# Optimization experiments

Hardware: AMD Instinct MI355X
Metric: run time of the kernel (lower is better)

## Reference

```python
import jax, jax.numpy as jnp
import numpy as np

QMIN, QMAX = -128.0, 127.0  # 8-bit signed activation range


def fq_act(x, s):
    """Fake-quantize activations: clip(round(x/s))*s with straight-through estimator."""
    y = jnp.clip(jnp.round(x / s), QMIN, QMAX) * s
    return x + jax.lax.stop_gradient(y - x)


def fq_weight(w):
    """Per-tensor max-abs symmetric (narrow-range) 8-bit weight fake-quant with STE."""
    s = jnp.max(jnp.abs(w)) / 127.0
    y = jnp.clip(jnp.round(w / s), -127.0, 127.0) * s
    return w + jax.lax.stop_gradient(y - w)


def conv1x1(x, w, b):
    # x: [b,c,h,w], w: [o,c] -> [b,o,h,w]
    return jnp.einsum('bchw,oc->bohw', x, w) + b[None, :, None, None]


def setup_inputs() -> dict:
    key = jax.random.key(0)
    ks = jax.random.split(key, 6)
    B, C, HC, H, W = 8, 64, 32, 64, 64
    x = jax.random.normal(ks[0], (B, C, H, W), dtype=jnp.float32)
    wq = jax.random.normal(ks[1], (HC, C), dtype=jnp.float32) * 0.05
    wk = jax.random.normal(ks[2], (HC, C), dtype=jnp.float32) * 0.05
    wv = jax.random.normal(ks[3], (HC, C), dtype=jnp.float32) * 0.05
    wp = jax.random.normal(ks[4], (C, HC), dtype=jnp.float32) * 0.05
    return {
        'x': x,
        'wq': wq, 'bq': jnp.zeros((HC,), jnp.float32),
        'wk': wk, 'bk': jnp.zeros((HC,), jnp.float32),
        'wv': wv, 'bv': jnp.zeros((HC,), jnp.float32),
        'wp': wp, 'bp': jnp.zeros((C,), jnp.float32),
        's_in': jnp.ones((1,), jnp.float32) * 0.0625,
        's_out': jnp.ones((1,), jnp.float32) * 0.0625,
    }


def reference(x, wq, bq, wk, bk, wv, bv, wp, bp, s_in, s_out):
    b, c, h, w = x.shape
    hc = wq.shape[0]
    n = h * w
    xq = fq_act(x, s_in)                              # quant_inp(x)
    q = conv1x1(xq, fq_weight(wq), bq).reshape(b, hc, n).transpose(0, 2, 1)  # [b,n,hc]
    k = conv1x1(xq, fq_weight(wk), bk).reshape(b, hc, n)                     # [b,hc,n]
    v = conv1x1(xq, fq_weight(wv), bv).reshape(b, hc, n).transpose(0, 2, 1)  # [b,n,hc]
    z = jax.nn.softmax(jnp.einsum('bqc,bck->bqk', q, k), axis=-1)            # [b,n,n]
    z = jnp.einsum('bqk,bkc->bqc', z, v).transpose(0, 2, 1).reshape(b, hc, h, w)
    z = fq_act(z, s_in)                               # quant_inp(z) (shared module/scale)
    out = xq + conv1x1(z, fq_weight(wp), bp)
    return fq_act(out, s_out)                         # self.act QuantIdentity
```

## Files before the change

### kernel.cpp

```cpp
#include <hip/hip_runtime.h>
#include <hip/hip_bf16.h>
#include <cstdint>
#include <cstddef>

#define NB 8
#define NC 64
#define NHC 32
#define NN 4096
#define LOG2E 1.44269504088896340736f

typedef short v8s __attribute__((ext_vector_type(8)));
typedef float v4f __attribute__((ext_vector_type(4)));

__device__ __forceinline__ unsigned short f2b(float f) {
    unsigned int u = __builtin_bit_cast(unsigned int, f);
    u += 0x7fffu + ((u >> 16) & 1u);
    return (unsigned short)(u >> 16);
}
__device__ __forceinline__ float b2f(unsigned short s) {
    unsigned int u = ((unsigned int)s) << 16;
    return __builtin_bit_cast(float, u);
}
__device__ __forceinline__ unsigned int pack2_bf16(float a, float b) {
    unsigned int ua = __builtin_bit_cast(unsigned int, a);
    ua += 0x7fffu + ((ua >> 16) & 1u);
    unsigned int ub = __builtin_bit_cast(unsigned int, b);
    ub += 0x7fffu + ((ub >> 16) & 1u);
    return (ua >> 16) | (ub & 0xffff0000u);
}
__device__ __forceinline__ unsigned int trunc2_bf16(float a, float b) {
    return __builtin_amdgcn_perm(__builtin_bit_cast(unsigned int, b),
                                 __builtin_bit_cast(unsigned int, a), 0x07060302u);
}

__global__ __launch_bounds__(256) void k_qkv(
    const float* __restrict__ x,
    const float* __restrict__ wq, const float* __restrict__ wk, const float* __restrict__ wv,
    const float* __restrict__ bq, const float* __restrict__ bk, const float* __restrict__ bv,
    const float* __restrict__ s_in,
    unsigned short* __restrict__ xqb, unsigned short* __restrict__ qb,
    unsigned short* __restrict__ kb, unsigned short* __restrict__ vb)
{
    int blk = blockIdx.x;
    int b   = blk >> 6;
    int p0  = (blk & 63) * 64;
    int tid = threadIdx.x;

    __shared__ __align__(16) unsigned short xt[64][72];
    __shared__ __align__(16) unsigned short wlds[6144];
    __shared__ float red[3][256];

    float4 q0 = *(const float4*)(wq + tid * 8), q1 = *(const float4*)(wq + tid * 8 + 4);
    float4 k0 = *(const float4*)(wk + tid * 8), k1 = *(const float4*)(wk + tid * 8 + 4);
    float4 v0 = *(const float4*)(wv + tid * 8), v1 = *(const float4*)(wv + tid * 8 + 4);
    float mq = fmaxf(fmaxf(fmaxf(fabsf(q0.x), fabsf(q0.y)), fmaxf(fabsf(q0.z), fabsf(q0.w))),
                     fmaxf(fmaxf(fabsf(q1.x), fabsf(q1.y)), fmaxf(fabsf(q1.z), fabsf(q1.w))));
    float mk = fmaxf(fmaxf(fmaxf(fabsf(k0.x), fabsf(k0.y)), fmaxf(fabsf(k0.z), fabsf(k0.w))),
                     fmaxf(fmaxf(fabsf(k1.x), fabsf(k1.y)), fmaxf(fabsf(k1.z), fabsf(k1.w))));
    float mv = fmaxf(fmaxf(fmaxf(fabsf(v0.x), fabsf(v0.y)), fmaxf(fabsf(v0.z), fabsf(v0.w))),
                     fmaxf(fmaxf(fabsf(v1.x), fabsf(v1.y)), fmaxf(fabsf(v1.z), fabsf(v1.w))));
    red[0][tid] = mq; red[1][tid] = mk; red[2][tid] = mv;
    __syncthreads();
    for (int s = 128; s > 0; s >>= 1) {
        if (tid < s) {
            red[0][tid] = fmaxf(red[0][tid], red[0][tid + s]);
            red[1][tid] = fmaxf(red[1][tid], red[1][tid + s]);
            red[2][tid] = fmaxf(red[2][tid], red[2][tid + s]);
        }
        __syncthreads();
    }
    float sq = red[0][0] / 127.0f, sk = red[1][0] / 127.0f, sw = red[2][0] / 127.0f;
    {
        const float* srcs[3] = {wq, wk, wv};
        float scl[3] = {sq, sk, sw};
        #pragma unroll
        for (int t = 0; t < 3; ++t) {
            #pragma unroll
            for (int j = 0; j < 8; ++j) {
                float val = srcs[t][tid * 8 + j];
                float r = fminf(fmaxf(rintf(val / scl[t]), -127.f), 127.f);
                wlds[t * 2048 + tid * 8 + j] = f2b(r * scl[t]);
            }
        }
    }

    float sv = s_in[0];
    float sinv = 1.0f / sv;
    int jj = tid & 15;
    int c0 = tid >> 4;
    #pragma unroll
    for (int it = 0; it < 4; ++it) {
        int c = c0 + it * 16;
        size_t gi = ((size_t)(b * NC + c) << 12) + p0 + jj * 4;
        float4 xv = *(const float4*)(x + gi);
        float r0 = fminf(fmaxf(rintf(xv.x * sinv), -128.f), 127.f) * sv;
        float r1 = fminf(fmaxf(rintf(xv.y * sinv), -128.f), 127.f) * sv;
        float r2 = fminf(fmaxf(rintf(xv.z * sinv), -128.f), 127.f) * sv;
        float r3 = fminf(fmaxf(rintf(xv.w * sinv), -128.f), 127.f) * sv;
        *(uint2*)(xqb + gi) = make_uint2(pack2_bf16(r0, r1), pack2_bf16(r2, r3));
        xt[jj * 4 + 0][c] = f2b(r0);
        xt[jj * 4 + 1][c] = f2b(r1);
        xt[jj * 4 + 2][c] = f2b(r2);
        xt[jj * 4 + 3][c] = f2b(r3);
    }
    __syncthreads();

    int wave = tid >> 6;
    int lane = tid & 63;
    int quad = lane >> 4;
    int l15  = lane & 15;

    v8s bf0 = *(const v8s*)(&xt[wave * 16 + l15][0  + quad * 8]);
    v8s bf1 = *(const v8s*)(&xt[wave * 16 + l15][32 + quad * 8]);

    int pos = p0 + wave * 16 + l15;
    size_t posg = (size_t)b * NN + pos;
    const v4f zc = {0.f, 0.f, 0.f, 0.f};

    #pragma unroll
    for (int rb = 0; rb < 6; ++rb) {
        v8s a0 = *(const v8s*)(wlds + (rb * 16 + l15) * 64 + 0  + quad * 8);
        v8s a1 = *(const v8s*)(wlds + (rb * 16 + l15) * 64 + 32 + quad * 8);
        v4f t   = __builtin_amdgcn_mfma_f32_16x16x32_bf16(a0, bf0, zc, 0, 0, 0);
        v4f acc = __builtin_amdgcn_mfma_f32_16x16x32_bf16(a1, bf1, t, 0, 0, 0);

        int R0 = rb * 16 + quad * 4;
        float vals[4];
        #pragma unroll
        for (int r = 0; r < 4; ++r) {
            int R = R0 + r;
            float bias = (R < 32) ? bq[R] : (R < 64) ? bk[R - 32] : bv[R - 64];
            float vv = acc[r] + bias;
            if (R < 32) vv *= LOG2E;
            vals[r] = vv;
        }
        if (R0 < 32) {
            *(unsigned int*)(qb + posg * NHC + R0)     = pack2_bf16(vals[0], vals[1]);
            *(unsigned int*)(qb + posg * NHC + R0 + 2) = pack2_bf16(vals[2], vals[3]);
        } else if (R0 < 64) {
            *(unsigned int*)(kb + posg * NHC + R0 - 32)     = pack2_bf16(vals[0], vals[1]);
            *(unsigned int*)(kb + posg * NHC + R0 - 32 + 2) = pack2_bf16(vals[2], vals[3]);
        } else {
            #pragma unroll
            for (int r = 0; r < 4; ++r)
                vb[(size_t)(b * NHC + R0 - 64 + r) * NN + pos] = f2b(vals[r]);
        }
    }
}

__global__ __launch_bounds__(256, 2) void k_attn(
    const unsigned short* __restrict__ qb, const unsigned short* __restrict__ kb,
    const unsigned short* __restrict__ vb, const unsigned short* __restrict__ xqb,
    const float* __restrict__ wp, const float* __restrict__ bp,
    const float* __restrict__ s_in, const float* __restrict__ s_out,
    float* __restrict__ out)
{
    int blk  = blockIdx.x;
    int b    = blk >> 6;
    int qt   = blk & 63;
    int qbase = qt * 64;
    int tid  = threadIdx.x;
    int wave = tid >> 6;
    int lane = tid & 63;
    int quad = lane >> 4;
    int l15  = lane & 15;

    __shared__ __align__(16) unsigned short pbuf[4][16 * 72];
    __shared__ __align__(16) float zbuf[4][64][36];
    __shared__ float lbuf[4][64];
    __shared__ __align__(16) unsigned short wpq[2048];
    __shared__ float red[256];

    {
        float4 a0 = *(const float4*)(wp + tid * 8), a1 = *(const float4*)(wp + tid * 8 + 4);
        float mx = fmaxf(fmaxf(fmaxf(fabsf(a0.x), fabsf(a0.y)), fmaxf(fabsf(a0.z), fabsf(a0.w))),
                         fmaxf(fmaxf(fabsf(a1.x), fabsf(a1.y)), fmaxf(fabsf(a1.z), fabsf(a1.w))));
        red[tid] = mx;
        __syncthreads();
        for (int s = 128; s > 0; s >>= 1) {
            if (tid < s) red[tid] = fmaxf(red[tid], red[tid + s]);
            __syncthreads();
        }
        float scale = red[0] / 127.0f;
        float e[8] = {a0.x, a0.y, a0.z, a0.w, a1.x, a1.y, a1.z, a1.w};
        #pragma unroll
        for (int j = 0; j < 8; ++j) {
            float r = fminf(fmaxf(rintf(e[j] / scale), -127.f), 127.f);
            wpq[tid * 8 + j] = f2b(r * scale);
        }
    }

    unsigned short* pb = pbuf[wave];
    const unsigned short* qbat = qb + (size_t)b * NN * NHC;
    const unsigned short* kbat = kb + (size_t)b * NN * NHC;
    const unsigned short* vbat = vb + (size_t)b * NHC * NN;

    v8s qf[4];
    #pragma unroll
    for (int s = 0; s < 4; ++s)
        qf[s] = *(const v8s*)(qbat + (qbase + s * 16 + l15) * NHC + quad * 8);

    const short one_bf16 = (short)0x3F80;
    const v8s ones = {one_bf16, one_bf16, one_bf16, one_bf16,
                      one_bf16, one_bf16, one_bf16, one_bf16};
    const v4f zc = {0.f, 0.f, 0.f, 0.f};
    v4f zt[4][2] = {{zc, zc}, {zc, zc}, {zc, zc}, {zc, zc}};
    v4f lacc[4] = {zc, zc, zc, zc};

    int k0 = wave * 1024;
    const unsigned short* vrow0 = vbat + (size_t)( 0 + l15) * NN;
    const unsigned short* vrow1 = vbat + (size_t)(16 + l15) * NN;

    v8s ck0 = *(const v8s*)(kbat + (k0 +  0 + l15) * NHC + quad * 8);
    v8s ck1 = *(const v8s*)(kbat + (k0 + 16 + l15) * NHC + quad * 8);
    v8s ck2 = *(const v8s*)(kbat + (k0 + 32 + l15) * NHC + quad * 8);
    v8s ck3 = *(const v8s*)(kbat + (k0 + 48 + l15) * NHC + quad * 8);

    for (int i = 0; i < 16; ++i) {
        int cki = k0 + (i << 6);
        int nki = k0 + (((i + 1) & 15) << 6);
        v8s nk0 = *(const v8s*)(kbat + (nki +  0 + l15) * NHC + quad * 8);
        v8s nk1 = *(const v8s*)(kbat + (nki + 16 + l15) * NHC + quad * 8);
        v8s nk2 = *(const v8s*)(kbat + (nki + 32 + l15) * NHC + quad * 8);
        v8s nk3 = *(const v8s*)(kbat + (nki + 48 + l15) * NHC + quad * 8);
        v8s cv0 = *(const v8s*)(vrow0 + cki +  0 + quad * 8);
        v8s cv1 = *(const v8s*)(vrow0 + cki + 32 + quad * 8);
        v8s cv2 = *(const v8s*)(vrow1 + cki +  0 + quad * 8);
        v8s cv3 = *(const v8s*)(vrow1 + cki + 32 + quad * 8);

        #pragma unroll
        for (int s = 0; s < 4; ++s) {
            v4f sa[4];
            sa[0] = __builtin_amdgcn_mfma_f32_16x16x32_bf16(ck0, qf[s], zc, 0, 0, 0);
            sa[1] = __builtin_amdgcn_mfma_f32_16x16x32_bf16(ck1, qf[s], zc, 0, 0, 0);
            sa[2] = __builtin_amdgcn_mfma_f32_16x16x32_bf16(ck2, qf[s], zc, 0, 0, 0);
            sa[3] = __builtin_amdgcn_mfma_f32_16x16x32_bf16(ck3, qf[s], zc, 0, 0, 0);

            #pragma unroll
            for (int t = 0; t < 4; ++t) {
                float p0 = __builtin_amdgcn_exp2f(sa[t][0]);
                float p1 = __builtin_amdgcn_exp2f(sa[t][1]);
                float p2 = __builtin_amdgcn_exp2f(sa[t][2]);
                float p3 = __builtin_amdgcn_exp2f(sa[t][3]);
                *(uint2*)(pb + l15 * 72 + 16 * t + quad * 4) =
                    make_uint2(trunc2_bf16(p0, p1), trunc2_bf16(p2, p3));
            }
            v8s pf0 = *(const v8s*)(pb + l15 * 72 +  0 + quad * 8);
            v8s pf1 = *(const v8s*)(pb + l15 * 72 + 32 + quad * 8);

            zt[s][0] = __builtin_amdgcn_mfma_f32_16x16x32_bf16(cv0, pf0, zt[s][0], 0, 0, 0);
            zt[s][0] = __builtin_amdgcn_mfma_f32_16x16x32_bf16(cv1, pf1, zt[s][0], 0, 0, 0);
            zt[s][1] = __builtin_amdgcn_mfma_f32_16x16x32_bf16(cv2, pf0, zt[s][1], 0, 0, 0);
            zt[s][1] = __builtin_amdgcn_mfma_f32_16x16x32_bf16(cv3, pf1, zt[s][1], 0, 0, 0);
            lacc[s]  = __builtin_amdgcn_mfma_f32_16x16x32_bf16(ones, pf0, lacc[s], 0, 0, 0);
            lacc[s]  = __builtin_amdgcn_mfma_f32_16x16x32_bf16(ones, pf1, lacc[s], 0, 0, 0);
        }
        ck0 = nk0; ck1 = nk1; ck2 = nk2; ck3 = nk3;
    }

    #pragma unroll
    for (int s = 0; s < 4; ++s) {
        *(v4f*)(&zbuf[wave][s * 16 + l15][     quad * 4]) = zt[s][0];
        *(v4f*)(&zbuf[wave][s * 16 + l15][16 + quad * 4]) = zt[s][1];
        if (quad == 0) lbuf[wave][s * 16 + l15] = lacc[s][0];
    }
    __syncthreads();

    int myq = wave * 16 + l15;
    float L = lbuf[0][myq] + lbuf[1][myq] + lbuf[2][myq] + lbuf[3][myq];

    float z[8] = {0.f};
    #pragma unroll
    for (int w = 0; w < 4; ++w) {
        v4f za  = *(const v4f*)(&zbuf[w][myq][quad * 8]);
        v4f zb2 = *(const v4f*)(&zbuf[w][myq][quad * 8 + 4]);
        #pragma unroll
        for (int j = 0; j < 4; ++j) { z[j] += za[j]; z[4 + j] += zb2[j]; }
    }
    float sv = s_in[0], sinv = 1.0f / sv;
    float so = s_out[0], soinv = 1.0f / so;
    float Linv = 1.0f / L;
    unsigned int zp[4];
    #pragma unroll
    for (int jp = 0; jp < 4; ++jp) {
        float a = z[2 * jp]     * Linv;
        float c = z[2 * jp + 1] * Linv;
        a = fminf(fmaxf(rintf(a * sinv), -128.f), 127.f) * sv;
        c = fminf(fmaxf(rintf(c * sinv), -128.f), 127.f) * sv;
        zp[jp] = pack2_bf16(a, c);
    }
    v8s zf = __builtin_bit_cast(v8s, *(uint4*)zp);

    v8s w0f = *(const v8s*)(wpq + ( 0 + l15) * NHC + quad * 8);
    v8s w1f = *(const v8s*)(wpq + (16 + l15) * NHC + quad * 8);
    v8s w2f = *(const v8s*)(wpq + (32 + l15) * NHC + quad * 8);
    v8s w3f = *(const v8s*)(wpq + (48 + l15) * NHC + quad * 8);
    v4f o0 = __builtin_amdgcn_mfma_f32_16x16x32_bf16(w0f, zf, zc, 0, 0, 0);
    v4f o1 = __builtin_amdgcn_mfma_f32_16x16x32_bf16(w1f, zf, zc, 0, 0, 0);
    v4f o2 = __builtin_amdgcn_mfma_f32_16x16x32_bf16(w2f, zf, zc, 0, 0, 0);
    v4f o3 = __builtin_amdgcn_mfma_f32_16x16x32_bf16(w3f, zf, zc, 0, 0, 0);

    int pos = qbase + wave * 16 + l15;
    #pragma unroll
    for (int ot = 0; ot < 4; ++ot) {
        v4f ov = (ot == 0) ? o0 : (ot == 1) ? o1 : (ot == 2) ? o2 : o3;
        #pragma unroll
        for (int r = 0; r < 4; ++r) {
            int oc = ot * 16 + quad * 4 + r;
            size_t idx = (size_t)(b * NC + oc) * NN + pos;
            float val = ov[r] + bp[oc] + b2f(xqb[idx]);
            float f = fminf(fmaxf(rintf(val * soinv), -128.f), 127.f);
            out[idx] = f * so;
        }
    }
}

extern "C" void kernel_launch(void* const* d_in, const int* in_sizes, int n_in,
                              void* d_out, int out_size, void* d_ws, size_t ws_size,
                              hipStream_t stream) {
    const float* x     = (const float*)d_in[0];
    const float* wq    = (const float*)d_in[1];
    const float* bq    = (const float*)d_in[2];
    const float* wk    = (const float*)d_in[3];
    const float* bk    = (const float*)d_in[4];
    const float* wv    = (const float*)d_in[5];
    const float* bv    = (const float*)d_in[6];
    const float* wp    = (const float*)d_in[7];
    const float* bp    = (const float*)d_in[8];
    const float* s_in  = (const float*)d_in[9];
    const float* s_out = (const float*)d_in[10];
    float* out = (float*)d_out;

    char* ws = (char*)d_ws;
    size_t off = 0;
    auto carve = [&](size_t bytes) {
        void* p = ws + off;
        off = (off + bytes + 255) & ~(size_t)255;
        return p;
    };
    unsigned short* xqb = (unsigned short*)carve((size_t)NB * NC * NN * 2);
    unsigned short* qbf = (unsigned short*)carve((size_t)NB * NN * NHC * 2);
    unsigned short* kbf = (unsigned short*)carve((size_t)NB * NN * NHC * 2);
    unsigned short* vbf = (unsigned short*)carve((size_t)NB * NHC * NN * 2);

    hipLaunchKernelGGL(k_qkv, dim3(512), dim3(256), 0, stream,
                       x, wq, wk, wv, bq, bk, bv, s_in, xqb, qbf, kbf, vbf);
    hipLaunchKernelGGL(k_attn, dim3(512), dim3(256), 0, stream,
                       qbf, kbf, vbf, xqb, wp, bp, s_in, s_out, out);
}
```

Baseline: 118.4 us.

## Feed softmax probabilities to PV MFMA from registers via permuted V layout

The attention kernel no longer stages the exponentiated scores through shared memory. It feeds each 16x16 score fragment directly as the B operand of 16x16x16 bf16 MFMAs, and the QKV kernel writes V with a permuted position order so the register layout matches. Block-wide max reductions for the weight scales now use wave shuffles instead of a shared-memory tree with many barriers. The explicit K prefetch double-buffering is removed, and the PV and row-sum work now runs as twice as many smaller MFMAs, which may expose more load latency.

```diff
diff --git a/kernel.cpp b/kernel.cpp
--- a/kernel.cpp
+++ b/kernel.cpp
@@ -10,7 +10,9 @@
 #define LOG2E 1.44269504088896340736f
 
 typedef short v8s __attribute__((ext_vector_type(8)));
+typedef short v4s __attribute__((ext_vector_type(4)));
 typedef float v4f __attribute__((ext_vector_type(4)));
+typedef unsigned int v2u __attribute__((ext_vector_type(2)));
 
 __device__ __forceinline__ unsigned short f2b(float f) {
     unsigned int u = __builtin_bit_cast(unsigned int, f);
@@ -31,6 +33,20 @@
 __device__ __forceinline__ unsigned int trunc2_bf16(float a, float b) {
     return __builtin_amdgcn_perm(__builtin_bit_cast(unsigned int, b),
                                  __builtin_bit_cast(unsigned int, a), 0x07060302u);
+}
+__device__ __forceinline__ float wave_max(float v) {
+    #pragma unroll
+    for (int off = 1; off < 64; off <<= 1) v = fmaxf(v, __shfl_xor(v, off));
+    return v;
+}
+__device__ __forceinline__ v4f mfma16bf16(v4s a, v4s b, v4f c) {
+#if __has_builtin(__builtin_amdgcn_mfma_f32_16x16x16bf16_1k)
+    return __builtin_amdgcn_mfma_f32_16x16x16bf16_1k(a, b, c, 0, 0, 0);
+#else
+    asm volatile("v_mfma_f32_16x16x16_bf16 %0, %1, %2, %0"
+                 : "+v"(c) : "v"(a), "v"(b));
+    return c;
+#endif
 }
 
 __global__ __launch_bounds__(256) void k_qkv(
@@ -45,10 +61,12 @@
     int b   = blk >> 6;
     int p0  = (blk & 63) * 64;
     int tid = threadIdx.x;
+    int wave = tid >> 6;
+    int lane = tid & 63;
 
     __shared__ __align__(16) unsigned short xt[64][72];
     __shared__ __align__(16) unsigned short wlds[6144];
-    __shared__ float red[3][256];
+    __shared__ float red[3][4];
 
     float4 q0 = *(const float4*)(wq + tid * 8), q1 = *(const float4*)(wq + tid * 8 + 4);
     float4 k0 = *(const float4*)(wk + tid * 8), k1 = *(const float4*)(wk + tid * 8 + 4);
@@ -59,28 +77,21 @@
                      fmaxf(fmaxf(fabsf(k1.x), fabsf(k1.y)), fmaxf(fabsf(k1.z), fabsf(k1.w))));
     float mv = fmaxf(fmaxf(fmaxf(fabsf(v0.x), fabsf(v0.y)), fmaxf(fabsf(v0.z), fabsf(v0.w))),
                      fmaxf(fmaxf(fabsf(v1.x), fabsf(v1.y)), fmaxf(fabsf(v1.z), fabsf(v1.w))));
-    red[0][tid] = mq; red[1][tid] = mk; red[2][tid] = mv;
+    mq = wave_max(mq); mk = wave_max(mk); mv = wave_max(mv);
+    if (lane == 0) { red[0][wave] = mq; red[1][wave] = mk; red[2][wave] = mv; }
     __syncthreads();
-    for (int s = 128; s > 0; s >>= 1) {
-        if (tid < s) {
-            red[0][tid] = fmaxf(red[0][tid], red[0][tid + s]);
-            red[1][tid] = fmaxf(red[1][tid], red[1][tid + s]);
-            red[2][tid] = fmaxf(red[2][tid], red[2][tid + s]);
-        }
-        __syncthreads();
-    }
-    float sq = red[0][0] / 127.0f, sk = red[1][0] / 127.0f, sw = red[2][0] / 127.0f;
+    float sq = fmaxf(fmaxf(red[0][0], red[0][1]), fmaxf(red[0][2], red[0][3])) / 127.0f;
+    float sk = fmaxf(fmaxf(red[1][0], red[1][1]), fmaxf(red[1][2], red[1][3])) / 127.0f;
+    float sw = fmaxf(fmaxf(red[2][0], red[2][1]), fmaxf(red[2][2], red[2][3])) / 127.0f;
     {
-        const float* srcs[3] = {wq, wk, wv};
-        float scl[3] = {sq, sk, sw};
-        #pragma unroll
-        for (int t = 0; t < 3; ++t) {
-            #pragma unroll
-            for (int j = 0; j < 8; ++j) {
-                float val = srcs[t][tid * 8 + j];
-                float r = fminf(fmaxf(rintf(val / scl[t]), -127.f), 127.f);
-                wlds[t * 2048 + tid * 8 + j] = f2b(r * scl[t]);
-            }
+        float eq[8] = {q0.x, q0.y, q0.z, q0.w, q1.x, q1.y, q1.z, q1.w};
+        float ek[8] = {k0.x, k0.y, k0.z, k0.w, k1.x, k1.y, k1.z, k1.w};
+        float ev[8] = {v0.x, v0.y, v0.z, v0.w, v1.x, v1.y, v1.z, v1.w};
+        #pragma unroll
+        for (int j = 0; j < 8; ++j) {
+            wlds[0 * 2048 + tid * 8 + j] = f2b(fminf(fmaxf(rintf(eq[j] / sq), -127.f), 127.f) * sq);
+            wlds[1 * 2048 + tid * 8 + j] = f2b(fminf(fmaxf(rintf(ek[j] / sk), -127.f), 127.f) * sk);
+            wlds[2 * 2048 + tid * 8 + j] = f2b(fminf(fmaxf(rintf(ev[j] / sw), -127.f), 127.f) * sw);
         }
     }
 
@@ -105,8 +116,6 @@
     }
     __syncthreads();
 
-    int wave = tid >> 6;
-    int lane = tid & 63;
     int quad = lane >> 4;
     int l15  = lane & 15;
 
@@ -115,6 +124,7 @@
 
     int pos = p0 + wave * 16 + l15;
     size_t posg = (size_t)b * NN + pos;
+    int posP = p0 + (l15 >> 2) * 16 + wave * 4 + (l15 & 3);
     const v4f zc = {0.f, 0.f, 0.f, 0.f};
 
     #pragma unroll
@@ -143,7 +153,7 @@
         } else {
             #pragma unroll
             for (int r = 0; r < 4; ++r)
-                vb[(size_t)(b * NHC + R0 - 64 + r) * NN + pos] = f2b(vals[r]);
+                vb[(size_t)(b * NHC + R0 - 64 + r) * NN + posP] = f2b(vals[r]);
         }
     }
 }
@@ -165,23 +175,19 @@
     int quad = lane >> 4;
     int l15  = lane & 15;
 
-    __shared__ __align__(16) unsigned short pbuf[4][16 * 72];
     __shared__ __align__(16) float zbuf[4][64][36];
     __shared__ float lbuf[4][64];
     __shared__ __align__(16) unsigned short wpq[2048];
-    __shared__ float red[256];
+    __shared__ float redw[4];
 
     {
         float4 a0 = *(const float4*)(wp + tid * 8), a1 = *(const float4*)(wp + tid * 8 + 4);
         float mx = fmaxf(fmaxf(fmaxf(fabsf(a0.x), fabsf(a0.y)), fmaxf(fabsf(a0.z), fabsf(a0.w))),
                          fmaxf(fmaxf(fabsf(a1.x), fabsf(a1.y)), fmaxf(fabsf(a1.z), fabsf(a1.w))));
-        red[tid] = mx;
+        mx = wave_max(mx);
+        if (lane == 0) redw[wave] = mx;
         __syncthreads();
-        for (int s = 128; s > 0; s >>= 1) {
-            if (tid < s) red[tid] = fmaxf(red[tid], red[tid + s]);
-            __syncthreads();
-        }
-        float scale = red[0] / 127.0f;
+        float scale = fmaxf(fmaxf(redw[0], redw[1]), fmaxf(redw[2], redw[3])) / 127.0f;
         float e[8] = {a0.x, a0.y, a0.z, a0.w, a1.x, a1.y, a1.z, a1.w};
         #pragma unroll
         for (int j = 0; j < 8; ++j) {
@@ -190,7 +196,6 @@
         }
     }
 
-    unsigned short* pb = pbuf[wave];
     const unsigned short* qbat = qb + (size_t)b * NN * NHC;
     const unsigned short* kbat = kb + (size_t)b * NN * NHC;
     const unsigned short* vbat = vb + (size_t)b * NHC * NN;
@@ -200,9 +205,8 @@
     for (int s = 0; s < 4; ++s)
         qf[s] = *(const v8s*)(qbat + (qbase + s * 16 + l15) * NHC + quad * 8);
 
-    const short one_bf16 = (short)0x3F80;
-    const v8s ones = {one_bf16, one_bf16, one_bf16, one_bf16,
-                      one_bf16, one_bf16, one_bf16, one_bf16};
+    const short ob = (short)0x3F80;
+    const v4s ones4 = {ob, ob, ob, ob};
     const v4f zc = {0.f, 0.f, 0.f, 0.f};
     v4f zt[4][2] = {{zc, zc}, {zc, zc}, {zc, zc}, {zc, zc}};
     v4f lacc[4] = {zc, zc, zc, zc};
@@ -211,22 +215,25 @@
     const unsigned short* vrow0 = vbat + (size_t)( 0 + l15) * NN;
     const unsigned short* vrow1 = vbat + (size_t)(16 + l15) * NN;
 
-    v8s ck0 = *(const v8s*)(kbat + (k0 +  0 + l15) * NHC + quad * 8);
-    v8s ck1 = *(const v8s*)(kbat + (k0 + 16 + l15) * NHC + quad * 8);
-    v8s ck2 = *(const v8s*)(kbat + (k0 + 32 + l15) * NHC + quad * 8);
-    v8s ck3 = *(const v8s*)(kbat + (k0 + 48 + l15) * NHC + quad * 8);
-
     for (int i = 0; i < 16; ++i) {
         int cki = k0 + (i << 6);
-        int nki = k0 + (((i + 1) & 15) << 6);
-        v8s nk0 = *(const v8s*)(kbat + (nki +  0 + l15) * NHC + quad * 8);
-        v8s nk1 = *(const v8s*)(kbat + (nki + 16 + l15) * NHC + quad * 8);
-        v8s nk2 = *(const v8s*)(kbat + (nki + 32 + l15) * NHC + quad * 8);
-        v8s nk3 = *(const v8s*)(kbat + (nki + 48 + l15) * NHC + quad * 8);
-        v8s cv0 = *(const v8s*)(vrow0 + cki +  0 + quad * 8);
-        v8s cv1 = *(const v8s*)(vrow0 + cki + 32 + quad * 8);
-        v8s cv2 = *(const v8s*)(vrow1 + cki +  0 + quad * 8);
-        v8s cv3 = *(const v8s*)(vrow1 + cki + 32 + quad * 8);
+        v8s ck0 = *(const v8s*)(kbat + (cki +  0 + l15) * NHC + quad * 8);
+        v8s ck1 = *(const v8s*)(kbat + (cki + 16 + l15) * NHC + quad * 8);
+        v8s ck2 = *(const v8s*)(kbat + (cki + 32 + l15) * NHC + quad * 8);
+        v8s ck3 = *(const v8s*)(kbat + (cki + 48 + l15) * NHC + quad * 8);
+        v8s v00 = *(const v8s*)(vrow0 + cki + quad * 16);
+        v8s v01 = *(const v8s*)(vrow0 + cki + quad * 16 + 8);
+        v8s v10 = *(const v8s*)(vrow1 + cki + quad * 16);
+        v8s v11 = *(const v8s*)(vrow1 + cki + quad * 16 + 8);
+        v4s va[2][4];
+        va[0][0] = __builtin_shufflevector(v00, v00, 0, 1, 2, 3);
+        va[0][1] = __builtin_shufflevector(v00, v00, 4, 5, 6, 7);
+        va[0][2] = __builtin_shufflevector(v01, v01, 0, 1, 2, 3);
+        va[0][3] = __builtin_shufflevector(v01, v01, 4, 5, 6, 7);
+        va[1][0] = __builtin_shufflevector(v10, v10, 0, 1, 2, 3);
+        va[1][1] = __builtin_shufflevector(v10, v10, 4, 5, 6, 7);
+        va[1][2] = __builtin_shufflevector(v11, v11, 0, 1, 2, 3);
+        va[1][3] = __builtin_shufflevector(v11, v11, 4, 5, 6, 7);
 
         #pragma unroll
         for (int s = 0; s < 4; ++s) {
@@ -238,24 +245,17 @@
 
             #pragma unroll
             for (int t = 0; t < 4; ++t) {
-                float p0 = __builtin_amdgcn_exp2f(sa[t][0]);
-                float p1 = __builtin_amdgcn_exp2f(sa[t][1]);
-                float p2 = __builtin_amdgcn_exp2f(sa[t][2]);
-                float p3 = __builtin_amdgcn_exp2f(sa[t][3]);
-                *(uint2*)(pb + l15 * 72 + 16 * t + quad * 4) =
-                    make_uint2(trunc2_bf16(p0, p1), trunc2_bf16(p2, p3));
+                v2u w;
+                w.x = trunc2_bf16(__builtin_amdgcn_exp2f(sa[t][0]),
+                                  __builtin_amdgcn_exp2f(sa[t][1]));
+                w.y = trunc2_bf16(__builtin_amdgcn_exp2f(sa[t][2]),
+                                  __builtin_amdgcn_exp2f(sa[t][3]));
+                v4s pfrag = __builtin_bit_cast(v4s, w);
+                zt[s][0] = mfma16bf16(va[0][t], pfrag, zt[s][0]);
+                zt[s][1] = mfma16bf16(va[1][t], pfrag, zt[s][1]);
+                lacc[s]  = mfma16bf16(ones4,    pfrag, lacc[s]);
             }
-            v8s pf0 = *(const v8s*)(pb + l15 * 72 +  0 + quad * 8);
-            v8s pf1 = *(const v8s*)(pb + l15 * 72 + 32 + quad * 8);
-
-            zt[s][0] = __builtin_amdgcn_mfma_f32_16x16x32_bf16(cv0, pf0, zt[s][0], 0, 0, 0);
-            zt[s][0] = __builtin_amdgcn_mfma_f32_16x16x32_bf16(cv1, pf1, zt[s][0], 0, 0, 0);
-            zt[s][1] = __builtin_amdgcn_mfma_f32_16x16x32_bf16(cv2, pf0, zt[s][1], 0, 0, 0);
-            zt[s][1] = __builtin_amdgcn_mfma_f32_16x16x32_bf16(cv3, pf1, zt[s][1], 0, 0, 0);
-            lacc[s]  = __builtin_amdgcn_mfma_f32_16x16x32_bf16(ones, pf0, lacc[s], 0, 0, 0);
-            lacc[s]  = __builtin_amdgcn_mfma_f32_16x16x32_bf16(ones, pf1, lacc[s], 0, 0, 0);
-        }
-        ck0 = nk0; ck1 = nk1; ck2 = nk2; ck3 = nk3;
+        }
     }
 
     #pragma unroll
```

Measured after the change: 112.6 us. -4.9%, faster.
